# Kernel optimization log

Measured on AMD Instinct MI355X. Metric: run time of the kernel, lower is better.

The kernel has to match this reference:

```python
import jax, jax.numpy as jnp
import numpy as np

N_NODES = 100000
F_STATE = 64
HIDDEN = 256
N_EDGES = 1600000


def setup_inputs() -> dict:
    key = jax.random.key(0)
    ks = jax.random.split(key, 8)
    x = jax.random.normal(ks[0], (N_NODES, F_STATE), dtype=jnp.float32)
    edge_index = jax.random.randint(ks[1], (2, N_EDGES), 0, N_NODES, dtype=jnp.int32)
    # Pre-process MLP (1 layer): Dense(F_STATE -> HIDDEN), relu
    W_pre = jax.random.normal(ks[2], (F_STATE, HIDDEN), dtype=jnp.float32) / np.sqrt(F_STATE)
    b_pre = jnp.zeros((HIDDEN,), dtype=jnp.float32)
    # GeneralConv: Dense(HIDDEN -> HIDDEN), relu, then sum-aggregate message passing
    W_conv = jax.random.normal(ks[3], (HIDDEN, HIDDEN), dtype=jnp.float32) / np.sqrt(HIDDEN)
    b_conv = jnp.zeros((HIDDEN,), dtype=jnp.float32)
    # Post-process MLP (1 layer): Dense(2*HIDDEN -> F_STATE), activation=None
    W_post = jax.random.normal(ks[4], (2 * HIDDEN, F_STATE), dtype=jnp.float32) / np.sqrt(2 * HIDDEN)
    b_post = jnp.zeros((F_STATE,), dtype=jnp.float32)
    return {
        "x": x,
        "edge_index": edge_index,
        "W_pre": W_pre,
        "b_pre": b_pre,
        "W_conv": W_conv,
        "b_conv": b_conv,
        "W_post": W_post,
        "b_post": b_post,
        "steps": 4,
    }


def reference(x, edge_index, W_pre, b_pre, W_conv, b_conv, W_post, b_post, steps):
    n = x.shape[0]
    dst = edge_index[0]  # a.indices[:, 0] -> aggregation targets
    src = edge_index[1]  # a.indices[:, 1] -> message sources

    def step(h, _):
        p = jax.nn.relu(h @ W_pre + b_pre)                 # pre MLP     [N, H]
        m = jax.nn.relu(p @ W_conv + b_conv)               # conv dense  [N, H]
        z = jax.ops.segment_sum(m[src], dst, num_segments=n)  # sum agg  [N, H]
        out = jnp.concatenate([z, p], axis=-1) @ W_post + b_post  # cat-skip + post MLP (linear)
        return out, None

    out, _ = jax.lax.scan(step, x, None, length=steps)
    return out
```

## Files before the change

### kernel.cpp

```cpp
#include <hip/hip_runtime.h>


#define NN 100000
#define NPAD 100064
#define FS 64
#define HH 256
#define NE 1600000
#define NSTEPS 4
#define GA 128
#define EPB (NE / GA)
#define BK2SH 9
#define NBK2 ((NN + 511) / 512)

typedef unsigned short u16;
typedef unsigned int u32;
typedef __attribute__((ext_vector_type(8))) short bfrag;
typedef __attribute__((ext_vector_type(4))) float ffrag;

static __device__ __forceinline__ u16 f2bf(float f) {
    union { float f; u32 u; } v; v.f = f;
    return (u16)((v.u + 0x7fffu + ((v.u >> 16) & 1u)) >> 16);
}
static __device__ __forceinline__ float bf2f(u16 h) {
    union { u32 u; float f; } v; v.u = (u32)h << 16; return v.f;
}
static __device__ __forceinline__ u32 pack2bf(float a, float b) {
    return (u32)f2bf(a) | ((u32)f2bf(b) << 16);
}

__global__ void cvt_x_k(const float4* __restrict__ x, uint2* __restrict__ hbf, int n4) {
    int i = blockIdx.x * 256 + threadIdx.x;
    if (i < n4) {
        float4 v = x[i];
        hbf[i] = make_uint2(pack2bf(v.x, v.y), pack2bf(v.z, v.w));
    }
}

template <int LK, int LC>
__global__ void transpose_cvt_k(const float* __restrict__ W, u16* __restrict__ Wt) {
    const int K = 1 << LK, C = 1 << LC;
    int i = blockIdx.x * 256 + threadIdx.x;
    if (i < K * C) {
        int c = i >> LK, k = i & (K - 1);
        Wt[i] = f2bf(W[(size_t)k * C + c]);
    }
}

__global__ void zero_int_k(int* __restrict__ p, int n) {
    int i = blockIdx.x * 256 + threadIdx.x;
    if (i < n) p[i] = 0;
}

__global__ void hist_k(const int* __restrict__ dst, int* __restrict__ cnt) {
    int e = blockIdx.x * 256 + threadIdx.x;
    if (e < NE) atomicAdd(&cnt[dst[e]], 1);
}

__global__ void scan1_k(const int* __restrict__ cnt, int* __restrict__ part, int* __restrict__ sums) {
    __shared__ int sh[256];
    const int t = threadIdx.x;
    const int base = blockIdx.x * 1024 + t * 4;
    int v0 = (base + 0 < NN) ? cnt[base + 0] : 0;
    int v1 = (base + 1 < NN) ? cnt[base + 1] : 0;
    int v2 = (base + 2 < NN) ? cnt[base + 2] : 0;
    int v3 = (base + 3 < NN) ? cnt[base + 3] : 0;
    int s = v0 + v1 + v2 + v3;
    sh[t] = s;
    __syncthreads();
    for (int o = 1; o < 256; o <<= 1) {
        int y = (t >= o) ? sh[t - o] : 0;
        __syncthreads();
        sh[t] += y;
        __syncthreads();
    }
    int ex = sh[t] - s;
    if (base + 0 < NN) part[base + 0] = ex; ex += v0;
    if (base + 1 < NN) part[base + 1] = ex; ex += v1;
    if (base + 2 < NN) part[base + 2] = ex; ex += v2;
    if (base + 3 < NN) part[base + 3] = ex;
    if (t == 0) sums[blockIdx.x] = sh[255];
}

__global__ void scan2_k(int* __restrict__ sums, int nb) {
    __shared__ int sh[128];
    const int t = threadIdx.x;
    int v = (t < nb) ? sums[t] : 0;
    sh[t] = v;
    __syncthreads();
    for (int o = 1; o < 128; o <<= 1) {
        int y = (t >= o) ? sh[t - o] : 0;
        __syncthreads();
        sh[t] += y;
        __syncthreads();
    }
    if (t < nb) sums[t] = sh[t] - v;
}

__global__ void scan3_k(int* __restrict__ offsets, const int* __restrict__ sums) {
    int i = blockIdx.x * 256 + threadIdx.x;
    if (i < NN) offsets[i] += sums[i >> 10];
}

__global__ void final_off_k(int* __restrict__ offsets) {
    if (threadIdx.x == 0) offsets[NN] = NE;
}

__global__ __launch_bounds__(256) void fillA_k(const int* __restrict__ dst, const int* __restrict__ src,
                                               int* __restrict__ cntM, int* __restrict__ offM,
                                               uint2* __restrict__ tmp) {
    __shared__ int cnt[256];
    __shared__ int sc[256];
    __shared__ int cur[256];
    const int t = threadIdx.x, b = blockIdx.x;
    const int e0 = b * EPB;
    cnt[t] = 0;
    __syncthreads();
    for (int i = t; i < EPB; i += 256) atomicAdd(&cnt[dst[e0 + i] >> BK2SH], 1);
    __syncthreads();
    int v = cnt[t];
    sc[t] = v;
    __syncthreads();
    for (int o = 1; o < 256; o <<= 1) {
        int y = (t >= o) ? sc[t - o] : 0;
        __syncthreads();
        sc[t] += y;
        __syncthreads();
    }
    int excl = sc[t] - v;
    cur[t] = excl;
    if (t < NBK2) {
        cntM[t * GA + b] = v;
        offM[t * GA + b] = excl;
    }
    __syncthreads();
    uint2* seg = tmp + (size_t)b * EPB;
    for (int i = t; i < EPB; i += 256) {
        int d = dst[e0 + i], s = src[e0 + i];
        int pos = atomicAdd(&cur[d >> BK2SH], 1);
        seg[pos] = make_uint2((u32)d, (u32)s);
    }
}

__global__ __launch_bounds__(256) void fillB_k(const uint2* __restrict__ tmp,
                                               const int* __restrict__ cntM, const int* __restrict__ offM,
                                               const int* __restrict__ offsets, int* __restrict__ srcs) {
    __shared__ int cur[512];
    __shared__ int runlen[GA];
    __shared__ int runoff[GA];
    const int t = threadIdx.x, k = blockIdx.x;
    const int nodeBase = k << BK2SH;
    for (int i = t; i < 512; i += 256) {
        int node = nodeBase + i;
        cur[i] = (node < NN) ? offsets[node] : 0;
    }
    if (t < GA) {
        runlen[t] = cntM[k * GA + t];
        runoff[t] = offM[k * GA + t];
    }
    __syncthreads();
    const int rsub = t >> 6;
    const int elane = t & 63;
    for (int g = 0; g < GA / 4; g++) {
        int rb = g * 4 + rsub;
        int len = runlen[rb];
        const uint2* run = tmp + (size_t)rb * EPB + runoff[rb];
        for (int e = elane; e < len; e += 64) {
            uint2 ed = run[e];
            int pos = atomicAdd(&cur[(int)ed.x - nodeBase], 1);
            srcs[pos] = (int)ed.y;
        }
    }
}

__global__ __launch_bounds__(256, 4) void xform_k(const u16* __restrict__ hbf,
                                                  const u16* __restrict__ Wpt,
                                                  const float* __restrict__ b_pre,
                                                  const u16* __restrict__ Wct,
                                                  const float* __restrict__ b_conv,
                                                  const u16* __restrict__ Wzt,
                                                  const u16* __restrict__ Wp2t,
                                                  u16* __restrict__ qbf,
                                                  float* __restrict__ pw2o) {
    __shared__ u16 ts[64 * 264];
    const int t = threadIdx.x;
    const int wave = t >> 6, lane = t & 63;
    const int quad = lane >> 4, l16 = lane & 15;
    const int nodeBase = blockIdx.x * 64;

    {
        ffrag acc[4][4];
#pragma unroll
        for (int mt = 0; mt < 4; mt++)
#pragma unroll
            for (int nt = 0; nt < 4; nt++) acc[mt][nt] = (ffrag)0.f;
#pragma unroll
        for (int ch = 0; ch < 2; ch++) {
            const int kb = ch * 32 + quad * 8;
            bfrag a[4], b[4];
#pragma unroll
            for (int mt = 0; mt < 4; mt++)
                a[mt] = *(const bfrag*)(hbf + (size_t)(nodeBase + mt * 16 + l16) * FS + kb);
#pragma unroll
            for (int nt = 0; nt < 4; nt++)
                b[nt] = *(const bfrag*)(Wpt + (size_t)(wave * 64 + nt * 16 + l16) * FS + kb);
#pragma unroll
            for (int mt = 0; mt < 4; mt++)
#pragma unroll
                for (int nt = 0; nt < 4; nt++)
                    acc[mt][nt] = __builtin_amdgcn_mfma_f32_16x16x32_bf16(a[mt], b[nt], acc[mt][nt], 0, 0, 0);
        }
#pragma unroll
        for (int nt = 0; nt < 4; nt++) {
            const int col = wave * 64 + nt * 16 + l16;
            const float bv = b_pre[col];
#pragma unroll
            for (int mt = 0; mt < 4; mt++)
#pragma unroll
                for (int r = 0; r < 4; r++)
                    ts[(mt * 16 + quad * 4 + r) * 264 + col] = f2bf(fmaxf(acc[mt][nt][r] + bv, 0.f));
        }
    }
    __syncthreads();

    ffrag accm[4][4];
    ffrag accw[4];
    {
#pragma unroll
        for (int mt = 0; mt < 4; mt++) {
            accw[mt] = (ffrag)0.f;
#pragma unroll
            for (int nt = 0; nt < 4; nt++) accm[mt][nt] = (ffrag)0.f;
        }
#pragma unroll
        for (int ch = 0; ch < 8; ch++) {
            const int kb = ch * 32 + quad * 8;
            bfrag a[4], b[4], bw;
#pragma unroll
            for (int mt = 0; mt < 4; mt++)
                a[mt] = *(const bfrag*)(ts + (mt * 16 + l16) * 264 + kb);
#pragma unroll
            for (int nt = 0; nt < 4; nt++)
                b[nt] = *(const bfrag*)(Wct + (size_t)(wave * 64 + nt * 16 + l16) * HH + kb);
            bw = *(const bfrag*)(Wp2t + (size_t)(wave * 16 + l16) * HH + kb);
#pragma unroll
            for (int mt = 0; mt < 4; mt++) {
#pragma unroll
                for (int nt = 0; nt < 4; nt++)
                    accm[mt][nt] = __builtin_amdgcn_mfma_f32_16x16x32_bf16(a[mt], b[nt], accm[mt][nt], 0, 0, 0);
                accw[mt] = __builtin_amdgcn_mfma_f32_16x16x32_bf16(a[mt], bw, accw[mt], 0, 0, 0);
            }
        }
    }
    __syncthreads();

    {
#pragma unroll
        for (int nt = 0; nt < 4; nt++) {
            const int col = wave * 64 + nt * 16 + l16;
            const float bv = b_conv[col];
#pragma unroll
            for (int mt = 0; mt < 4; mt++)
#pragma unroll
                for (int r = 0; r < 4; r++)
                    ts[(mt * 16 + quad * 4 + r) * 264 + col] = f2bf(fmaxf(accm[mt][nt][r] + bv, 0.f));
        }
        const int colw = wave * 16 + l16;
#pragma unroll
        for (int mt = 0; mt < 4; mt++)
#pragma unroll
            for (int r = 0; r < 4; r++) {
                int node = nodeBase + mt * 16 + quad * 4 + r;
                if (node < NN) pw2o[(size_t)node * FS + colw] = accw[mt][r];
            }
    }
    __syncthreads();

    {
        ffrag qa[4];
#pragma unroll
        for (int mt = 0; mt < 4; mt++) qa[mt] = (ffrag)0.f;
#pragma unroll
        for (int ch = 0; ch < 8; ch++) {
            const int kb = ch * 32 + quad * 8;
            bfrag bz = *(const bfrag*)(Wzt + (size_t)(wave * 16 + l16) * HH + kb);
#pragma unroll
            for (int mt = 0; mt < 4; mt++) {
                bfrag am = *(const bfrag*)(ts + (mt * 16 + l16) * 264 + kb);
                qa[mt] = __builtin_amdgcn_mfma_f32_16x16x32_bf16(am, bz, qa[mt], 0, 0, 0);
            }
        }
        const int col = wave * 16 + l16;
#pragma unroll
        for (int mt = 0; mt < 4; mt++)
#pragma unroll
            for (int r = 0; r < 4; r++) {
                int node = nodeBase + mt * 16 + quad * 4 + r;
                if (node < NN) qbf[(size_t)node * FS + col] = f2bf(qa[mt][r]);
            }
    }
}

__global__ __launch_bounds__(256) void agg_k(const u32* __restrict__ q2,
                                             const int* __restrict__ offsets,
                                             const int* __restrict__ srcs,
                                             const float* __restrict__ pw2,
                                             const float* __restrict__ b_post,
                                             u32* __restrict__ hbf_out,
                                             float* __restrict__ outf) {
    const int wave = threadIdx.x >> 6;
    const int lane = threadIdx.x & 63;
    const int node = blockIdx.x * 4 + wave;
    const int half = lane >> 5, c = lane & 31;
    const int beg = offsets[node], end = offsets[node + 1];
    float ax = 0.f, ay = 0.f, bx = 0.f, by = 0.f;
    int e = beg + half;
    for (; e + 6 < end; e += 8) {
        int s0 = srcs[e], s1 = srcs[e + 2], s2 = srcs[e + 4], s3 = srcs[e + 6];
        u32 g0 = q2[(size_t)s0 * 32 + c];
        u32 g1 = q2[(size_t)s1 * 32 + c];
        u32 g2 = q2[(size_t)s2 * 32 + c];
        u32 g3 = q2[(size_t)s3 * 32 + c];
        ax += bf2f((u16)g0) + bf2f((u16)g1);
        ay += bf2f((u16)(g0 >> 16)) + bf2f((u16)(g1 >> 16));
        bx += bf2f((u16)g2) + bf2f((u16)g3);
        by += bf2f((u16)(g2 >> 16)) + bf2f((u16)(g3 >> 16));
    }
    for (; e < end; e += 2) {
        u32 g = q2[(size_t)srcs[e] * 32 + c];
        ax += bf2f((u16)g);
        ay += bf2f((u16)(g >> 16));
    }
    ax += bx; ay += by;
    ax += __shfl_xor(ax, 32);
    ay += __shfl_xor(ay, 32);
    if (half == 0) {
        float2 w = *(const float2*)&pw2[(size_t)node * FS + 2 * c];
        float2 b = *(const float2*)&b_post[2 * c];
        float hx = ax + w.x + b.x;
        float hy = ay + w.y + b.y;
        if (outf) {
            *(float2*)&outf[(size_t)node * FS + 2 * c] = make_float2(hx, hy);
        } else {
            hbf_out[(size_t)node * 32 + c] = pack2bf(hx, hy);
        }
    }
}

extern "C" void kernel_launch(void* const* d_in, const int* in_sizes, int n_in,
                              void* d_out, int out_size, void* d_ws, size_t ws_size,
                              hipStream_t stream) {
    const float* x      = (const float*)d_in[0];
    const int*   ei     = (const int*)d_in[1];
    const float* W_pre  = (const float*)d_in[2];
    const float* b_pre  = (const float*)d_in[3];
    const float* W_conv = (const float*)d_in[4];
    const float* b_conv = (const float*)d_in[5];
    const float* W_post = (const float*)d_in[6];
    const float* b_post = (const float*)d_in[7];
    float* out = (float*)d_out;

    char* ws = (char*)d_ws;
    size_t off = 0;
    auto alloc = [&](size_t bytes) -> char* {
        char* r = ws + off;
        off += (bytes + 255) & ~(size_t)255;
        return r;
    };
    u16* hbf     = (u16*)alloc((size_t)NPAD * FS * 2);
    u16* qbf     = (u16*)alloc((size_t)NN * FS * 2);
    float* pw2   = (float*)alloc((size_t)NPAD * FS * 4);
    uint2* tmp   = (uint2*)alloc((size_t)NE * 8);
    int* offsets = (int*)alloc((size_t)(NN + 1) * 4);
    int* cnt     = (int*)alloc((size_t)NN * 4);
    int* srcs    = (int*)alloc((size_t)NE * 4);
    int* sums    = (int*)alloc(128 * 4);
    int* cntM    = (int*)alloc((size_t)NBK2 * GA * 4);
    int* offM    = (int*)alloc((size_t)NBK2 * GA * 4);
    u16* Wpt     = (u16*)alloc((size_t)HH * FS * 2);
    u16* Wct     = (u16*)alloc((size_t)HH * HH * 2);
    u16* Wzt     = (u16*)alloc((size_t)FS * HH * 2);
    u16* Wp2t    = (u16*)alloc((size_t)FS * HH * 2);
    (void)ws_size; (void)in_sizes; (void)n_in; (void)out_size;

    const int* dst = ei;
    const int* src = ei + NE;

    cvt_x_k<<<(NN * FS / 4 + 255) / 256, 256, 0, stream>>>((const float4*)x, (uint2*)hbf, NN * FS / 4);
    transpose_cvt_k<6, 8><<<(HH * FS + 255) / 256, 256, 0, stream>>>(W_pre, Wpt);
    transpose_cvt_k<8, 8><<<(HH * HH + 255) / 256, 256, 0, stream>>>(W_conv, Wct);
    transpose_cvt_k<8, 6><<<(HH * FS + 255) / 256, 256, 0, stream>>>(W_post, Wzt);
    transpose_cvt_k<8, 6><<<(HH * FS + 255) / 256, 256, 0, stream>>>(W_post + HH * FS, Wp2t);

    zero_int_k<<<(NN + 255) / 256, 256, 0, stream>>>(cnt, NN);
    hist_k<<<(NE + 255) / 256, 256, 0, stream>>>(dst, cnt);
    const int NB = (NN + 1023) / 1024;
    scan1_k<<<NB, 256, 0, stream>>>(cnt, offsets, sums);
    scan2_k<<<1, 128, 0, stream>>>(sums, NB);
    scan3_k<<<(NN + 255) / 256, 256, 0, stream>>>(offsets, sums);
    final_off_k<<<1, 64, 0, stream>>>(offsets);

    fillA_k<<<GA, 256, 0, stream>>>(dst, src, cntM, offM, tmp);
    fillB_k<<<NBK2, 256, 0, stream>>>(tmp, cntM, offM, offsets, srcs);

    const int GB = (NN + 63) / 64;
    for (int s = 0; s < NSTEPS; s++) {
        xform_k<<<GB, 256, 0, stream>>>(hbf, Wpt, b_pre, Wct, b_conv, Wzt, Wp2t, qbf, pw2);
        if (s < NSTEPS - 1)
            agg_k<<<NN / 4, 256, 0, stream>>>((const u32*)qbf, offsets, srcs, pw2, b_post,
                                              (u32*)hbf, nullptr);
        else
            agg_k<<<NN / 4, 256, 0, stream>>>((const u32*)qbf, offsets, srcs, pw2, b_post,
                                              nullptr, out);
    }
}
```

Measured before the change: 706.5 us.

## Build CSR offsets inside bucket fill and fuse weight prep kernels

Removes the global histogram with atomics and the three-kernel scan by computing per-node counts and offsets inside fillB from the bucketed edges, using a small bucket-level scan kernel. It also packs each edge's local destination and source into one 32-bit word, halving temporary traffic, and merges the four weight transpose kernels into one launch. This cuts many small launches and global atomics from preprocessing. In exchange fillB reads its runs twice, and the packing relies on source indices fitting in 23 bits.

```diff
diff --git a/kernel.cpp b/kernel.cpp
--- a/kernel.cpp
+++ b/kernel.cpp
@@ -10,7 +10,8 @@
 #define GA 128
 #define EPB (NE / GA)
 #define BK2SH 9
-#define NBK2 ((NN + 511) / 512)
+#define BS2 (1 << BK2SH)
+#define NBK2 ((NN + BS2 - 1) / BS2)
 
 typedef unsigned short u16;
 typedef unsigned int u32;
@@ -36,78 +37,32 @@
     }
 }
 
-template <int LK, int LC>
-__global__ void transpose_cvt_k(const float* __restrict__ W, u16* __restrict__ Wt) {
-    const int K = 1 << LK, C = 1 << LC;
+__global__ void prep_w_k(const float* __restrict__ W_pre, const float* __restrict__ W_conv,
+                         const float* __restrict__ W_post,
+                         u16* __restrict__ Wpt, u16* __restrict__ Wct,
+                         u16* __restrict__ Wzt, u16* __restrict__ Wp2t) {
     int i = blockIdx.x * 256 + threadIdx.x;
-    if (i < K * C) {
-        int c = i >> LK, k = i & (K - 1);
-        Wt[i] = f2bf(W[(size_t)k * C + c]);
-    }
-}
-
-__global__ void zero_int_k(int* __restrict__ p, int n) {
-    int i = blockIdx.x * 256 + threadIdx.x;
-    if (i < n) p[i] = 0;
-}
-
-__global__ void hist_k(const int* __restrict__ dst, int* __restrict__ cnt) {
-    int e = blockIdx.x * 256 + threadIdx.x;
-    if (e < NE) atomicAdd(&cnt[dst[e]], 1);
-}
-
-__global__ void scan1_k(const int* __restrict__ cnt, int* __restrict__ part, int* __restrict__ sums) {
-    __shared__ int sh[256];
-    const int t = threadIdx.x;
-    const int base = blockIdx.x * 1024 + t * 4;
-    int v0 = (base + 0 < NN) ? cnt[base + 0] : 0;
-    int v1 = (base + 1 < NN) ? cnt[base + 1] : 0;
-    int v2 = (base + 2 < NN) ? cnt[base + 2] : 0;
-    int v3 = (base + 3 < NN) ? cnt[base + 3] : 0;
-    int s = v0 + v1 + v2 + v3;
-    sh[t] = s;
-    __syncthreads();
-    for (int o = 1; o < 256; o <<= 1) {
-        int y = (t >= o) ? sh[t - o] : 0;
-        __syncthreads();
-        sh[t] += y;
-        __syncthreads();
-    }
-    int ex = sh[t] - s;
-    if (base + 0 < NN) part[base + 0] = ex; ex += v0;
-    if (base + 1 < NN) part[base + 1] = ex; ex += v1;
-    if (base + 2 < NN) part[base + 2] = ex; ex += v2;
-    if (base + 3 < NN) part[base + 3] = ex;
-    if (t == 0) sums[blockIdx.x] = sh[255];
-}
-
-__global__ void scan2_k(int* __restrict__ sums, int nb) {
-    __shared__ int sh[128];
-    const int t = threadIdx.x;
-    int v = (t < nb) ? sums[t] : 0;
-    sh[t] = v;
-    __syncthreads();
-    for (int o = 1; o < 128; o <<= 1) {
-        int y = (t >= o) ? sh[t - o] : 0;
-        __syncthreads();
-        sh[t] += y;
-        __syncthreads();
-    }
-    if (t < nb) sums[t] = sh[t] - v;
-}
-
-__global__ void scan3_k(int* __restrict__ offsets, const int* __restrict__ sums) {
-    int i = blockIdx.x * 256 + threadIdx.x;
-    if (i < NN) offsets[i] += sums[i >> 10];
-}
-
-__global__ void final_off_k(int* __restrict__ offsets) {
-    if (threadIdx.x == 0) offsets[NN] = NE;
+    if (i < 65536) {
+        int c = i >> 8, k = i & 255;
+        Wct[i] = f2bf(W_conv[k * HH + c]);
+    } else if (i < 81920) {
+        int j = i - 65536;
+        int c = j >> 6, k = j & 63;
+        Wpt[j] = f2bf(W_pre[k * HH + c]);
+    } else if (i < 98304) {
+        int j = i - 81920;
+        int c = j >> 8, k = j & 255;
+        Wzt[j] = f2bf(W_post[k * FS + c]);
+    } else if (i < 114688) {
+        int j = i - 98304;
+        int c = j >> 8, k = j & 255;
+        Wp2t[j] = f2bf(W_post[(HH + k) * FS + c]);
+    }
 }
 
 __global__ __launch_bounds__(256) void fillA_k(const int* __restrict__ dst, const int* __restrict__ src,
                                                int* __restrict__ cntM, int* __restrict__ offM,
-                                               uint2* __restrict__ tmp) {
+                                               u32* __restrict__ tmp) {
     __shared__ int cnt[256];
     __shared__ int sc[256];
     __shared__ int cur[256];
@@ -133,26 +88,44 @@
         offM[t * GA + b] = excl;
     }
     __syncthreads();
-    uint2* seg = tmp + (size_t)b * EPB;
+    u32* seg = tmp + (size_t)b * EPB;
     for (int i = t; i < EPB; i += 256) {
         int d = dst[e0 + i], s = src[e0 + i];
         int pos = atomicAdd(&cur[d >> BK2SH], 1);
-        seg[pos] = make_uint2((u32)d, (u32)s);
-    }
-}
-
-__global__ __launch_bounds__(256) void fillB_k(const uint2* __restrict__ tmp,
+        seg[pos] = ((u32)(d & (BS2 - 1)) << 23) | (u32)s;
+    }
+}
+
+__global__ void bscan_k(const int* __restrict__ cntM, int* __restrict__ bstart) {
+    __shared__ int sh[256];
+    const int t = threadIdx.x;
+    int tot = 0;
+    if (t < NBK2)
+        for (int b = 0; b < GA; b++) tot += cntM[t * GA + b];
+    sh[t] = tot;
+    __syncthreads();
+    for (int o = 1; o < 256; o <<= 1) {
+        int y = (t >= o) ? sh[t - o] : 0;
+        __syncthreads();
+        sh[t] += y;
+        __syncthreads();
+    }
+    if (t < NBK2) bstart[t] = sh[t] - tot;
+    if (t == 255) bstart[NBK2] = sh[255];
+}
+
+__global__ __launch_bounds__(256) void fillB_k(const u32* __restrict__ tmp,
                                                const int* __restrict__ cntM, const int* __restrict__ offM,
-                                               const int* __restrict__ offsets, int* __restrict__ srcs) {
-    __shared__ int cur[512];
+                                               const int* __restrict__ bstart,
+                                               int* __restrict__ offsets, int* __restrict__ srcs) {
+    __shared__ int cnt[BS2];
+    __shared__ int cur[BS2];
     __shared__ int runlen[GA];
     __shared__ int runoff[GA];
     const int t = threadIdx.x, k = blockIdx.x;
     const int nodeBase = k << BK2SH;
-    for (int i = t; i < 512; i += 256) {
-        int node = nodeBase + i;
-        cur[i] = (node < NN) ? offsets[node] : 0;
-    }
+    cnt[t] = 0;
+    cnt[t + 256] = 0;
     if (t < GA) {
         runlen[t] = cntM[k * GA + t];
         runoff[t] = offM[k * GA + t];
@@ -163,13 +136,45 @@
     for (int g = 0; g < GA / 4; g++) {
         int rb = g * 4 + rsub;
         int len = runlen[rb];
-        const uint2* run = tmp + (size_t)rb * EPB + runoff[rb];
+        const u32* run = tmp + (size_t)rb * EPB + runoff[rb];
+        for (int e = elane; e < len; e += 64) atomicAdd(&cnt[run[e] >> 23], 1);
+    }
+    __syncthreads();
+    int a = cnt[2 * t], b2 = cnt[2 * t + 1];
+    int s = a + b2;
+    cur[t] = s;
+    __syncthreads();
+    for (int o = 1; o < 256; o <<= 1) {
+        int y = (t >= o) ? cur[t - o] : 0;
+        __syncthreads();
+        cur[t] += y;
+        __syncthreads();
+    }
+    int exclPair = cur[t] - s;
+    __syncthreads();
+    const int base = bstart[k];
+    int o0 = base + exclPair;
+    int o1 = o0 + a;
+    int n0 = nodeBase + 2 * t, n1 = n0 + 1;
+    if (n0 < NN) offsets[n0] = o0;
+    if (n1 < NN) offsets[n1] = o1;
+    cur[2 * t] = o0;
+    cur[2 * t + 1] = o1;
+    __syncthreads();
+    for (int g = 0; g < GA / 4; g++) {
+        int rb = g * 4 + rsub;
+        int len = runlen[rb];
+        const u32* run = tmp + (size_t)rb * EPB + runoff[rb];
         for (int e = elane; e < len; e += 64) {
-            uint2 ed = run[e];
-            int pos = atomicAdd(&cur[(int)ed.x - nodeBase], 1);
-            srcs[pos] = (int)ed.y;
-        }
-    }
+            u32 p = run[e];
+            int pos = atomicAdd(&cur[p >> 23], 1);
+            srcs[pos] = (int)(p & 0x7FFFFFu);
+        }
+    }
+}
+
+__global__ void final_off_k(int* __restrict__ offsets) {
+    if (threadIdx.x == 0) offsets[NN] = NE;
 }
 
 __global__ __launch_bounds__(256, 4) void xform_k(const u16* __restrict__ hbf,
@@ -369,13 +374,12 @@
     u16* hbf     = (u16*)alloc((size_t)NPAD * FS * 2);
     u16* qbf     = (u16*)alloc((size_t)NN * FS * 2);
     float* pw2   = (float*)alloc((size_t)NPAD * FS * 4);
-    uint2* tmp   = (uint2*)alloc((size_t)NE * 8);
+    u32* tmp     = (u32*)alloc((size_t)NE * 4);
     int* offsets = (int*)alloc((size_t)(NN + 1) * 4);
-    int* cnt     = (int*)alloc((size_t)NN * 4);
     int* srcs    = (int*)alloc((size_t)NE * 4);
-    int* sums    = (int*)alloc(128 * 4);
     int* cntM    = (int*)alloc((size_t)NBK2 * GA * 4);
     int* offM    = (int*)alloc((size_t)NBK2 * GA * 4);
+    int* bstart  = (int*)alloc((size_t)(NBK2 + 1) * 4);
     u16* Wpt     = (u16*)alloc((size_t)HH * FS * 2);
     u16* Wct     = (u16*)alloc((size_t)HH * HH * 2);
     u16* Wzt     = (u16*)alloc((size_t)FS * HH * 2);
@@ -386,21 +390,12 @@
     const int* src = ei + NE;
 
     cvt_x_k<<<(NN * FS / 4 + 255) / 256, 256, 0, stream>>>((const float4*)x, (uint2*)hbf, NN * FS / 4);
-    transpose_cvt_k<6, 8><<<(HH * FS + 255) / 256, 256, 0, stream>>>(W_pre, Wpt);
-    transpose_cvt_k<8, 8><<<(HH * HH + 255) / 256, 256, 0, stream>>>(W_conv, Wct);
-    transpose_cvt_k<8, 6><<<(HH * FS + 255) / 256, 256, 0, stream>>>(W_post, Wzt);
-    transpose_cvt_k<8, 6><<<(HH * FS + 255) / 256, 256, 0, stream>>>(W_post + HH * FS, Wp2t);
-
-    zero_int_k<<<(NN + 255) / 256, 256, 0, stream>>>(cnt, NN);
-    hist_k<<<(NE + 255) / 256, 256, 0, stream>>>(dst, cnt);
-    const int NB = (NN + 1023) / 1024;
-    scan1_k<<<NB, 256, 0, stream>>>(cnt, offsets, sums);
-    scan2_k<<<1, 128, 0, stream>>>(sums, NB);
-    scan3_k<<<(NN + 255) / 256, 256, 0, stream>>>(offsets, sums);
+    prep_w_k<<<448, 256, 0, stream>>>(W_pre, W_conv, W_post, Wpt, Wct, Wzt, Wp2t);
+
+    fillA_k<<<GA, 256, 0, stream>>>(dst, src, cntM, offM, tmp);
+    bscan_k<<<1, 256, 0, stream>>>(cntM, bstart);
+    fillB_k<<<NBK2, 256, 0, stream>>>(tmp, cntM, offM, bstart, offsets, srcs);
     final_off_k<<<1, 64, 0, stream>>>(offsets);
-
-    fillA_k<<<GA, 256, 0, stream>>>(dst, src, cntM, offM, tmp);
-    fillB_k<<<NBK2, 256, 0, stream>>>(tmp, cntM, offM, offsets, srcs);
 
     const int GB = (NN + 63) / 64;
     for (int s = 0; s < NSTEPS; s++) {
```

Measured after the change: 641.6 us. 9.2% less time.
